# Optimization experiments

Hardware: AMD Instinct MI355X
Metric: run time of the kernel (lower is better)

Reference implementation:

```python
import jax, jax.numpy as jnp
import numpy as np

D = 2048      # d_model
BASE = 10000  # RoPE base
B = 16        # batch of (D, D) inputs


def setup_inputs() -> dict:
    key = jax.random.key(0)
    x_m = jax.random.normal(key, (B, D, D), dtype=jnp.float32)
    return {"x_m": x_m, "m": 7}


def _rotation_matrix(m):
    # inverse[i] = 1 / base**(2*i/d), i in [0, d/2)
    half = D // 2
    inv = 1.0 / (BASE ** (2.0 * jnp.arange(half, dtype=jnp.float32) / D))
    ang = m * inv                      # (d/2,)
    c, s = jnp.cos(ang), jnp.sin(ang)
    ev = 2 * jnp.arange(half)          # even row/col indices
    R = jnp.zeros((D, D), dtype=jnp.float32)
    # 2x2 block-diagonal rotation matrix, same layout as the torch loop
    R = (R.at[ev, ev].set(c)
          .at[ev + 1, ev + 1].set(c)
          .at[ev, ev + 1].set(-s)
          .at[ev + 1, ev].set(s))
    return R


def reference(x_m, m):
    # Faithful to the original: ELEMENTWISE product r_theta * x_m
    # (the torch code uses `*`, not `@`), broadcasting R over the batch.
    R = _rotation_matrix(jnp.float32(m))   # (D, D)
    return R * x_m                          # (B, D, D)
```

## Files before the change

### kernel.cpp

```cpp
#include <hip/hip_runtime.h>
#include <math.h>


constexpr int D = 2048;
constexpr int B = 16;
constexpr long long TOTAL4 = (long long)B * D * D / 4;

__global__ __launch_bounds__(256) void rope_block_diag_kernel(
        const float* __restrict__ x, const int* __restrict__ m_ptr,
        float* __restrict__ out) {
    const long long idx = (long long)blockIdx.x * blockDim.x + threadIdx.x;
    const int col4 = (int)(idx & (D / 4 - 1));
    const int j0   = col4 << 2;
    const int i    = (int)((idx >> 9) & (D - 1));

    float4 v = make_float4(0.f, 0.f, 0.f, 0.f);

    if (j0 == (i & ~3)) {
        const int m = *m_ptr;
        const int p = i >> 1;
        const double ang = (double)m * exp((-2.0 * (double)p / (double)D) * log(10000.0));
        const float c = (float)cos(ang);
        const float s = (float)sin(ang);

        const float4 xv = ((const float4*)x)[idx];
        const int o = i & 2;
        const float xa = (o == 0) ? xv.x : xv.z;
        const float xb = (o == 0) ? xv.y : xv.w;
        const float va = (i & 1) ? (s * xa) : (c * xa);
        const float vb = (i & 1) ? (c * xb) : (-s * xb);
        if (o == 0) { v.x = va; v.y = vb; }
        else        { v.z = va; v.w = vb; }
    }

    ((float4*)out)[idx] = v;
}

extern "C" void kernel_launch(void* const* d_in, const int* in_sizes, int n_in,
                              void* d_out, int out_size, void* d_ws, size_t ws_size,
                              hipStream_t stream) {
    const float* x     = (const float*)d_in[0];
    const int*   m_ptr = (const int*)d_in[1];
    float*       out   = (float*)d_out;

    const int block = 256;
    const long long grid = TOTAL4 / block;
    rope_block_diag_kernel<<<(unsigned)grid, block, 0, stream>>>(x, m_ptr, out);
}
```

Baseline: 369.2 us.

## Zero output with memset and patch only diagonal 2x2 blocks

Replaces the full-tensor elementwise kernel with a hipMemsetAsync that zero-fills the output, followed by a small kernel that writes only the 2x2 rotation blocks on each row's diagonal. This removes the per-element index checks and divergent trig work from the bulk write path and lets the runtime fill routine handle the zeros. It adds a second launch and strided scattered float2 accesses in the patch kernel.

```diff
diff --git a/kernel.cpp b/kernel.cpp
--- a/kernel.cpp
+++ b/kernel.cpp
@@ -4,36 +4,32 @@
 
 constexpr int D = 2048;
 constexpr int B = 16;
-constexpr long long TOTAL4 = (long long)B * D * D / 4;
 
-__global__ __launch_bounds__(256) void rope_block_diag_kernel(
+__global__ __launch_bounds__(256) void rope_patch_kernel(
         const float* __restrict__ x, const int* __restrict__ m_ptr,
         float* __restrict__ out) {
-    const long long idx = (long long)blockIdx.x * blockDim.x + threadIdx.x;
-    const int col4 = (int)(idx & (D / 4 - 1));
-    const int j0   = col4 << 2;
-    const int i    = (int)((idx >> 9) & (D - 1));
+    const int t = blockIdx.x * blockDim.x + threadIdx.x;
+    const int i  = t & (D - 1);
+    const int c0 = i & ~1;
+    const int p  = i >> 1;
 
-    float4 v = make_float4(0.f, 0.f, 0.f, 0.f);
+    const int m = *m_ptr;
+    const double ang = (double)m * exp((-2.0 * (double)p / (double)D) * log(10000.0));
+    const float c = (float)cos(ang);
+    const float s = (float)sin(ang);
 
-    if (j0 == (i & ~3)) {
-        const int m = *m_ptr;
-        const int p = i >> 1;
-        const double ang = (double)m * exp((-2.0 * (double)p / (double)D) * log(10000.0));
-        const float c = (float)cos(ang);
-        const float s = (float)sin(ang);
+    const long long base = (long long)t * D + c0;
+    const float2 xv = *(const float2*)(x + base);
 
-        const float4 xv = ((const float4*)x)[idx];
-        const int o = i & 2;
-        const float xa = (o == 0) ? xv.x : xv.z;
-        const float xb = (o == 0) ? xv.y : xv.w;
-        const float va = (i & 1) ? (s * xa) : (c * xa);
-        const float vb = (i & 1) ? (c * xb) : (-s * xb);
-        if (o == 0) { v.x = va; v.y = vb; }
-        else        { v.z = va; v.w = vb; }
+    float2 v;
+    if (i & 1) {
+        v.x = s * xv.x;
+        v.y = c * xv.y;
+    } else {
+        v.x = c * xv.x;
+        v.y = -s * xv.y;
     }
-
-    ((float4*)out)[idx] = v;
+    *(float2*)(out + base) = v;
 }
 
 extern "C" void kernel_launch(void* const* d_in, const int* in_sizes, int n_in,
@@ -43,7 +39,9 @@
     const int*   m_ptr = (const int*)d_in[1];
     float*       out   = (float*)d_out;
 
+    hipMemsetAsync(d_out, 0, (size_t)B * D * D * sizeof(float), stream);
+
     const int block = 256;
-    const long long grid = TOTAL4 / block;
-    rope_block_diag_kernel<<<(unsigned)grid, block, 0, stream>>>(x, m_ptr, out);
+    const int grid  = (B * D) / block;
+    rope_patch_kernel<<<grid, block, 0, stream>>>(x, m_ptr, out);
 }
```

After: 374.4 us. Within noise of the previous version (+1.4%).
